# Kernel optimization log

Measured on AMD Instinct MI355X. Metric: run time of the kernel, lower is better.

Reference implementation:

```python
import jax, jax.numpy as jnp
import numpy as np

B, N, D = 4, 4096, 768
H, DH = 12, 64          # heads, dim_head; inner_dim = H*DH = D
DEPTH = 4
HID = int(D * 4.0)      # mlp hidden
LN_EPS = 1e-5


def setup_inputs() -> dict:
    key = jax.random.key(0)
    ks = jax.random.split(key, 7)
    s = 0.02
    return {
        "x": jax.random.normal(ks[0], (B, N, D), jnp.float32),
        "ln1_g": jnp.ones((DEPTH, D), jnp.float32),
        "ln1_b": jnp.zeros((DEPTH, D), jnp.float32),
        "qkv_w": jax.random.normal(ks[1], (DEPTH, D, H * DH), jnp.float32) * s,
        "temp": jnp.ones((DEPTH, H, 1), jnp.float32),
        "out_w": jax.random.normal(ks[2], (DEPTH, H * DH, D), jnp.float32) * s,
        "out_b": jnp.zeros((DEPTH, D), jnp.float32),
        "ln2_g": jnp.ones((DEPTH, D), jnp.float32),
        "ln2_b": jnp.zeros((DEPTH, D), jnp.float32),
        "fc1_w": jax.random.normal(ks[3], (DEPTH, D, HID), jnp.float32) * s,
        "fc1_b": jnp.zeros((DEPTH, HID), jnp.float32),
        "fc2_w": jax.random.normal(ks[4], (DEPTH, HID, D), jnp.float32) * s,
        "fc2_b": jnp.zeros((DEPTH, D), jnp.float32),
    }


def _layernorm(x, g, b):
    mu = jnp.mean(x, axis=-1, keepdims=True)
    var = jnp.mean((x - mu) ** 2, axis=-1, keepdims=True)
    return (x - mu) * jax.lax.rsqrt(var + LN_EPS) * g + b


def _tss_attention(h, qkv_w, temp, out_w, out_b):
    b, n, d = h.shape
    w = h @ qkv_w                                   # (b, n, H*DH)
    w = w.reshape(b, n, H, DH).transpose(0, 2, 1, 3)  # (b, h, n, d)
    # F.normalize over token dim (dim=-2), eps=1e-12
    nrm = jnp.sqrt(jnp.sum(w * w, axis=2, keepdims=True))
    w_normed = w / jnp.maximum(nrm, 1e-12)
    logits = jnp.sum(w_normed * w_normed, axis=-1) * temp[None]  # (b, h, n)
    Pi = jax.nn.softmax(logits, axis=-1)
    Pi_n = Pi / (jnp.sum(Pi, axis=-1, keepdims=True) + 1e-8)
    dots = jnp.einsum('bhn,bhnd->bhd', Pi_n, w * w)[:, :, None, :]  # (b, h, 1, d)
    attn = 1.0 / (1.0 + dots)
    out = -(w * Pi[..., None]) * attn               # (b, h, n, d)
    out = out.transpose(0, 2, 1, 3).reshape(b, n, H * DH)
    return out @ out_w + out_b


def reference(x, ln1_g, ln1_b, qkv_w, temp, out_w, out_b,
              ln2_g, ln2_b, fc1_w, fc1_b, fc2_w, fc2_b):
    for i in range(DEPTH):
        h = _layernorm(x, ln1_g[i], ln1_b[i])
        x = _tss_attention(h, qkv_w[i], temp[i], out_w[i], out_b[i]) + x
        h2 = _layernorm(x, ln2_g[i], ln2_b[i])
        mlp = jax.nn.gelu(h2 @ fc1_w[i] + fc1_b[i], approximate=False) @ fc2_w[i] + fc2_b[i]
        x = mlp + x
    return x
```

## Files before the change

### kernel.cpp

```cpp
#include <hip/hip_runtime.h>
#include <cstdint>
#include <cstddef>

static constexpr int Bc = 4, Nc = 4096, Dc = 768, Hc = 12, DHc = 64;
static constexpr int HIDc = 3072, DEPTHc = 4;
static constexpr int Mc = Bc * Nc;
static constexpr int BHc = Bc * Hc;
static constexpr int BHDc = BHc * DHc;

typedef unsigned short u16;
typedef __bf16 bf16x8 __attribute__((ext_vector_type(8)));
typedef float  f32x4  __attribute__((ext_vector_type(4)));

#define DEV __device__ __forceinline__

DEV u16 f2bf(float x) {
    uint32_t u = __float_as_uint(x);
    u += 0x7fffu + ((u >> 16) & 1u);
    return (u16)(u >> 16);
}
DEV float bf2f(u16 u) { return __uint_as_float(((uint32_t)u) << 16); }
DEV void unp2(uint32_t u, float& a, float& b) {
    a = __uint_as_float(u << 16);
    b = __uint_as_float(u & 0xffff0000u);
}
DEV float gelu_fast(float x) {
    float y = 0.7978845608f * (x + 0.044715f * x * x * x);
    float e = __expf(2.0f * y);
    float t = 1.0f - 2.0f / (e + 1.0f);
    return 0.5f * x * (1.0f + t);
}

DEV void ldg_lds16(const void* g, void* l) {
    __builtin_amdgcn_global_load_lds(
        (const __attribute__((address_space(1))) uint32_t*)(uintptr_t)g,
        (__attribute__((address_space(3))) uint32_t*)(uint32_t)(uintptr_t)l,
        16, 0, 0);
}

__global__ void detect_kernel(const uint32_t* __restrict__ x, uint32_t* __restrict__ flag) {
    int t = threadIdx.x;
    uint32_t w = x[t];
    int e = (w >> 7) & 0xFF;
    __shared__ int cnt[256];
    cnt[t] = (e >= 100 && e <= 140) ? 1 : 0;
    __syncthreads();
    for (int s = 128; s; s >>= 1) {
        if (t < s) cnt[t] += cnt[t + s];
        __syncthreads();
    }
    if (t == 0) flag[0] = (cnt[0] >= 128) ? 1u : 0u;
}

__global__ __launch_bounds__(256) void sentinel_kernel(u16* __restrict__ out, int n) {
    int i = blockIdx.x * 256 + threadIdx.x;
    if (i < n) out[i] = 0x449A;
}

__global__ __launch_bounds__(256) void cvt_param_kernel(
    const void* __restrict__ src, float* __restrict__ dst, int n,
    const uint32_t* __restrict__ flag) {
    int i = blockIdx.x * 256 + threadIdx.x;
    if (i >= n) return;
    if (flag[0]) dst[i] = bf2f(((const u16*)src)[i]);
    else         dst[i] = ((const float*)src)[i];
}

__global__ __launch_bounds__(256) void transpose_cvt_off(
    const void* __restrict__ src, size_t eoff, u16* __restrict__ dst,
    int R, int C, const uint32_t* __restrict__ flag) {
    __shared__ u16 tile[32][33];
    const bool isbf = (flag[0] != 0);
    int c0 = blockIdx.x * 32, r0 = blockIdx.y * 32;
    int tx = threadIdx.x & 31, ty = threadIdx.x >> 5;
#pragma unroll
    for (int j = 0; j < 32; j += 8) {
        size_t off = eoff + (size_t)(r0 + ty + j) * C + (c0 + tx);
        tile[ty + j][tx] = isbf ? ((const u16*)src)[off] : f2bf(((const float*)src)[off]);
    }
    __syncthreads();
#pragma unroll
    for (int j = 0; j < 32; j += 8)
        dst[(size_t)(c0 + ty + j) * R + (r0 + tx)] = tile[tx][ty + j];
}

__global__ __launch_bounds__(256) void ln_kernel(
    const float* __restrict__ x, const float* __restrict__ g,
    const float* __restrict__ bta, u16* __restrict__ out) {
    int row = blockIdx.x, t = threadIdx.x;
    const float* xr = x + (size_t)row * Dc;
    float v0 = xr[t], v1 = xr[t + 256], v2 = xr[t + 512];
    float s = v0 + v1 + v2;
    float ss = v0 * v0 + v1 * v1 + v2 * v2;
    __shared__ float red[8];
    for (int m = 32; m; m >>= 1) { s += __shfl_xor(s, m, 64); ss += __shfl_xor(ss, m, 64); }
    int wave = t >> 6, lane = t & 63;
    if (lane == 0) { red[wave] = s; red[4 + wave] = ss; }
    __syncthreads();
    s  = red[0] + red[1] + red[2] + red[3];
    ss = red[4] + red[5] + red[6] + red[7];
    float mu = s * (1.0f / Dc);
    float var = ss * (1.0f / Dc) - mu * mu;
    float rs = rsqrtf(var + 1e-5f);
    u16* orow = out + (size_t)row * Dc;
    orow[t]       = f2bf((v0 - mu) * rs * g[t]       + bta[t]);
    orow[t + 256] = f2bf((v1 - mu) * rs * g[t + 256] + bta[t + 256]);
    orow[t + 512] = f2bf((v2 - mu) * rs * g[t + 512] + bta[t + 512]);
}

template <int MODE>
__global__ __launch_bounds__(512, 2) void gemm_kernel(
    const u16* __restrict__ A, const u16* __restrict__ Bt,
    float* Cf, u16* Cb, const float* __restrict__ bias, const float* res,
    float* aux, int M, int N, int K) {
    __shared__ __attribute__((aligned(16))) u16 lds[2][2][2][256 * 32];
    const int tid = threadIdx.x;
    const int wave = tid >> 6, lane = tid & 63;
    const int wm = wave >> 2, wn = wave & 3;
    const int bm = blockIdx.y * 256, bn = blockIdx.x * 256;
    const int NKS = K >> 6;

    u16* Lm = &lds[0][0][0][0];
    const u16* L = Lm;

    const int schunk = (lane & 3) ^ ((lane >> 3) & 3);
    const u16* ag = A  + (size_t)(bm + wave * 16 + (lane >> 2)) * K + schunk * 8;
    const u16* bg = Bt + (size_t)(bn + wave * 16 + (lane >> 2)) * K + schunk * 8;
    const size_t jstep = (size_t)128 * K;

    const int fm = lane & 15, fc = lane >> 4;
    const int chunk = (fc ^ ((fm >> 1) & 3)) * 8;
    const int aE0 = (wm * 128 + fm) * 32 + chunk;
    const int aE1 = 8192 + aE0;
    const int bE0 = 32768 + (wn * 64 + fm) * 32 + chunk;
    const int bE1 = 8192 + bE0;

    f32x4 acc[8][4] = {};
    bf16x8 afr[8], bq[2], bq2[2];

#define STG(OP, GB, SS, DD, KH)                                              \
    {   const u16* g_ = GB + (size_t)(SS) * 64 + (KH) * 32;                  \
        u16* d_ = Lm + (OP) * 32768 + (DD) * 16384 + (KH) * 8192 + wave * 512; \
        ldg_lds16(g_, d_);                                                   \
        ldg_lds16(g_ + jstep, d_ + 4096); }

#define MF2(NB, BQ)                                                          \
    __builtin_amdgcn_s_setprio(1);                                           \
    _Pragma("unroll")                                                        \
    for (int m = 0; m < 8; ++m) {                                            \
        acc[m][(NB)]     = __builtin_amdgcn_mfma_f32_16x16x32_bf16(          \
            afr[m], BQ[0], acc[m][(NB)], 0, 0, 0);                           \
        acc[m][(NB) + 1] = __builtin_amdgcn_mfma_f32_16x16x32_bf16(          \
            afr[m], BQ[1], acc[m][(NB) + 1], 0, 0, 0);                       \
    }                                                                        \
    __builtin_amdgcn_s_setprio(0);

#define SYNC                                                                 \
    __builtin_amdgcn_s_barrier();                                            \
    asm volatile("s_waitcnt lgkmcnt(0)" ::: "memory");                       \
    __builtin_amdgcn_sched_barrier(0);

#define VM4 asm volatile("s_waitcnt vmcnt(4)" ::: "memory");

#define KSTEP(D, SS1) {                                                      \
    \
    _Pragma("unroll")                                                        \
    for (int m = 0; m < 8; ++m)                                              \
        afr[m] = *(const bf16x8*)(L + (D) * 16384 + aE0 + m * 512);          \
    bq[0] = *(const bf16x8*)(L + (D) * 16384 + bE0);                         \
    bq[1] = *(const bf16x8*)(L + (D) * 16384 + bE0 + 512);                   \
    STG(0, ag, SS1, (D) ^ 1, 0);                                             \
    SYNC;                                                                    \
    MF2(0, bq);                                                              \
    \
    bq2[0] = *(const bf16x8*)(L + (D) * 16384 + bE0 + 1024);                 \
    bq2[1] = *(const bf16x8*)(L + (D) * 16384 + bE0 + 1536);                 \
    STG(1, bg, SS1, (D) ^ 1, 0);                                             \
    VM4;                                                                     \
    SYNC;                                                                    \
    MF2(2, bq2);                                                             \
    \
    _Pragma("unroll")                                                        \
    for (int m = 0; m < 8; ++m)                                              \
        afr[m] = *(const bf16x8*)(L + (D) * 16384 + aE1 + m * 512);          \
    bq2[0] = *(const bf16x8*)(L + (D) * 16384 + bE1 + 1024);                 \
    bq2[1] = *(const bf16x8*)(L + (D) * 16384 + bE1 + 1536);                 \
    STG(0, ag, SS1, (D) ^ 1, 1);                                             \
    SYNC;                                                                    \
    MF2(2, bq2);                                                             \
    \
    bq[0] = *(const bf16x8*)(L + (D) * 16384 + bE1);                         \
    bq[1] = *(const bf16x8*)(L + (D) * 16384 + bE1 + 512);                   \
    STG(1, bg, SS1, (D) ^ 1, 1);                                             \
    VM4;                                                                     \
    SYNC;                                                                    \
    MF2(0, bq);                                                              \
}

    STG(0, ag, 0, 0, 0);
    STG(1, bg, 0, 0, 0);
    STG(0, ag, 0, 0, 1);
    STG(1, bg, 0, 0, 1);
    asm volatile("s_waitcnt vmcnt(4)" ::: "memory");
    __builtin_amdgcn_s_barrier();
    __builtin_amdgcn_sched_barrier(0);

    for (int s = 0; s < NKS; s += 2) {
        KSTEP(0, s + 1);
        const int s2 = (s + 2 < NKS) ? s + 2 : 0;
        KSTEP(1, s2);
    }
    asm volatile("s_waitcnt vmcnt(0)" ::: "memory");

#undef KSTEP
#undef VM4
#undef SYNC
#undef MF2
#undef STG

    const int er = (lane >> 4) * 4;
    const int ec = lane & 15;
    float csq[4] = {0.f, 0.f, 0.f, 0.f};
#pragma unroll
    for (int mf = 0; mf < 8; ++mf) {
        const int row0 = bm + wm * 128 + mf * 16 + er;
#pragma unroll
        for (int nf = 0; nf < 4; ++nf) {
            const int col = bn + wn * 64 + nf * 16 + ec;
#pragma unroll
            for (int r = 0; r < 4; ++r) {
                const size_t off = (size_t)(row0 + r) * N + col;
                float v = acc[mf][nf][r];
                if (MODE == 1) {
                    Cf[off] = v + bias[col] + res[off];
                } else if (MODE == 2) {
                    Cb[off] = f2bf(gelu_fast(v + bias[col]));
                } else {
                    Cb[off] = f2bf(v);
                    csq[nf] += v * v;
                }
            }
        }
    }
    if (MODE == 3) {
        const int b = bm >> 12;
#pragma unroll
        for (int nf = 0; nf < 4; ++nf) {
            float s = csq[nf];
            s += __shfl_xor(s, 16, 64);
            s += __shfl_xor(s, 32, 64);
            if (lane < 16) {
                const int col = bn + wn * 64 + nf * 16 + lane;
                const int bh = b * Hc + (col >> 6);
                atomicAdd(&aux[bh * DHc + (col & 63)], s);
            }
        }
    }
}

__global__ __launch_bounds__(256) void logits_kernel(
    const u16* __restrict__ w, const float* __restrict__ nrm2,
    const float* __restrict__ tp, float* __restrict__ logits) {
    int blk = blockIdx.x;
    int chunk = blk & 15, bh = blk >> 4;
    int b = bh / Hc, h = bh - b * Hc;
    int t = threadIdx.x, dq = t & 3, nr = t >> 2;
    __shared__ float inv[64];
    if (t < 64) inv[t] = 1.0f / fmaxf(nrm2[bh * DHc + t], 1e-24f);
    __syncthreads();
    float tl = tp[h];
#pragma unroll
    for (int jj = 0; jj < 4; jj++) {
        int n = chunk * 256 + jj * 64 + nr;
        const uint4* wr = (const uint4*)(w + ((size_t)b * Nc + n) * Dc + h * DHc + dq * 16);
        uint4 u0 = wr[0], u1 = wr[1];
        float acc = 0.f;
        float e0, e1;
        const float* iv = inv + dq * 16;
        unp2(u0.x, e0, e1); acc += e0 * e0 * iv[0]  + e1 * e1 * iv[1];
        unp2(u0.y, e0, e1); acc += e0 * e0 * iv[2]  + e1 * e1 * iv[3];
        unp2(u0.z, e0, e1); acc += e0 * e0 * iv[4]  + e1 * e1 * iv[5];
        unp2(u0.w, e0, e1); acc += e0 * e0 * iv[6]  + e1 * e1 * iv[7];
        unp2(u1.x, e0, e1); acc += e0 * e0 * iv[8]  + e1 * e1 * iv[9];
        unp2(u1.y, e0, e1); acc += e0 * e0 * iv[10] + e1 * e1 * iv[11];
        unp2(u1.z, e0, e1); acc += e0 * e0 * iv[12] + e1 * e1 * iv[13];
        unp2(u1.w, e0, e1); acc += e0 * e0 * iv[14] + e1 * e1 * iv[15];
        acc += __shfl_xor(acc, 1, 64);
        acc += __shfl_xor(acc, 2, 64);
        if (dq == 0) logits[(size_t)bh * Nc + n] = tl * acc;
    }
}

__global__ __launch_bounds__(256) void softmax_kernel(
    const float* __restrict__ logits, float* __restrict__ Pi, float* __restrict__ rowsc) {
    int bh = blockIdx.x, t = threadIdx.x;
    int wave = t >> 6, lane = t & 63;
    const float4* lg = (const float4*)(logits + (size_t)bh * Nc);
    float4 v[4];
    float mx = -3.4e38f;
    __shared__ float red[4];
#pragma unroll
    for (int j = 0; j < 4; j++) {
        v[j] = lg[t + 256 * j];
        mx = fmaxf(mx, fmaxf(fmaxf(v[j].x, v[j].y), fmaxf(v[j].z, v[j].w)));
    }
    for (int m = 32; m; m >>= 1) mx = fmaxf(mx, __shfl_xor(mx, m, 64));
    if (lane == 0) red[wave] = mx;
    __syncthreads();
    mx = fmaxf(fmaxf(red[0], red[1]), fmaxf(red[2], red[3]));
    __syncthreads();
    float s = 0.f;
#pragma unroll
    for (int j = 0; j < 4; j++) {
        v[j].x = expf(v[j].x - mx); v[j].y = expf(v[j].y - mx);
        v[j].z = expf(v[j].z - mx); v[j].w = expf(v[j].w - mx);
        s += v[j].x + v[j].y + v[j].z + v[j].w;
    }
    for (int m = 32; m; m >>= 1) s += __shfl_xor(s, m, 64);
    if (lane == 0) red[wave] = s;
    __syncthreads();
    s = red[0] + red[1] + red[2] + red[3];
    __syncthreads();
    float invs = 1.0f / s;
    float s2 = 0.f;
    float4* Pr = (float4*)(Pi + (size_t)bh * Nc);
#pragma unroll
    for (int j = 0; j < 4; j++) {
        float4 p;
        p.x = v[j].x * invs; p.y = v[j].y * invs;
        p.z = v[j].z * invs; p.w = v[j].w * invs;
        s2 += p.x + p.y + p.z + p.w;
        Pr[t + 256 * j] = p;
    }
    for (int m = 32; m; m >>= 1) s2 += __shfl_xor(s2, m, 64);
    if (lane == 0) red[wave] = s2;
    __syncthreads();
    if (t == 0) rowsc[bh] = 1.0f / (red[0] + red[1] + red[2] + red[3] + 1e-8f);
}

__global__ __launch_bounds__(256) void dots_kernel(
    const u16* __restrict__ w, const float* __restrict__ Pi,
    const float* __restrict__ rowsc, float* __restrict__ dots) {
    int blk = blockIdx.x;
    int chunk = blk & 15, bh = blk >> 4;
    int b = bh / Hc, h = bh - b * Hc;
    int t = threadIdx.x, d4 = t & 15, rg = t >> 4;
    const u16* base = w + ((size_t)b * Nc + chunk * 256 + rg) * Dc + h * DHc + d4 * 4;
    const float* Prow = Pi + (size_t)bh * Nc + chunk * 256 + rg;
    float4 acc = {0.f, 0.f, 0.f, 0.f};
#pragma unroll 4
    for (int j = 0; j < 16; j++) {
        uint2 u = *(const uint2*)(base + (size_t)j * 16 * Dc);
        float p = Prow[j * 16];
        float a0, a1, a2, a3;
        unp2(u.x, a0, a1); unp2(u.y, a2, a3);
        acc.x += p * a0 * a0; acc.y += p * a1 * a1;
        acc.z += p * a2 * a2; acc.w += p * a3 * a3;
    }
    __shared__ float4 red[256];
    red[t] = acc;
    __syncthreads();
    if (t < 64) {
        float s = 0.f;
#pragma unroll
        for (int r = 0; r < 16; r++) {
            const float* f = (const float*)&red[r * 16 + (t >> 2)];
            s += f[t & 3];
        }
        atomicAdd(&dots[bh * DHc + t], s * rowsc[bh]);
    }
}

__global__ __launch_bounds__(256) void attnout_kernel(
    const u16* __restrict__ w, const float* __restrict__ Pi,
    const float* __restrict__ dots, u16* __restrict__ out) {
    int idx = blockIdx.x * 256 + threadIdx.x;
    int cg = idx % (Dc / 8);
    int m = idx / (Dc / 8);
    int b = m >> 12, n = m & 4095;
    int c = cg * 8, h = c >> 6, d = c & 63;
    int bh = b * Hc + h;
    uint4 wv = ((const uint4*)w)[idx];
    float pi = Pi[(size_t)bh * Nc + n];
    float4 dv0 = *(const float4*)(dots + bh * DHc + d);
    float4 dv1 = *(const float4*)(dots + bh * DHc + d + 4);
    float a0, a1, a2, a3, a4, a5, a6, a7;
    unp2(wv.x, a0, a1); unp2(wv.y, a2, a3);
    unp2(wv.z, a4, a5); unp2(wv.w, a6, a7);
    union { u16 u[8]; uint4 v4; } pk;
    pk.u[0] = f2bf(-(a0 * pi) / (1.0f + dv0.x));
    pk.u[1] = f2bf(-(a1 * pi) / (1.0f + dv0.y));
    pk.u[2] = f2bf(-(a2 * pi) / (1.0f + dv0.z));
    pk.u[3] = f2bf(-(a3 * pi) / (1.0f + dv0.w));
    pk.u[4] = f2bf(-(a4 * pi) / (1.0f + dv1.x));
    pk.u[5] = f2bf(-(a5 * pi) / (1.0f + dv1.y));
    pk.u[6] = f2bf(-(a6 * pi) / (1.0f + dv1.z));
    pk.u[7] = f2bf(-(a7 * pi) / (1.0f + dv1.w));
    ((uint4*)out)[idx] = pk.v4;
}

extern "C" void kernel_launch(void* const* d_in, const int* in_sizes, int n_in,
                              void* d_out, int out_size, void* d_ws, size_t ws_size,
                              hipStream_t stream) {
    const void* x_in = d_in[0];
    const void* ln1g = d_in[1];
    const void* ln1b = d_in[2];
    const void* qkvw = d_in[3];
    const void* temp = d_in[4];
    const void* outw = d_in[5];
    const void* outb = d_in[6];
    const void* ln2g = d_in[7];
    const void* ln2b = d_in[8];
    const void* fc1w = d_in[9];
    const void* fc1b = d_in[10];
    const void* fc2w = d_in[11];
    const void* fc2b = d_in[12];

    char* p = (char*)d_ws;
    auto alloc = [&](size_t bytes) {
        void* r = (void*)p;
        p += (bytes + 255) & ~(size_t)255;
        return r;
    };
    float* xbuf = (float*)alloc((size_t)Mc * Dc * 4);
    void*  big  = alloc((size_t)Mc * HIDc * 2);
    u16*   wbuf = (u16*)big;
    u16*   gbuf = (u16*)big;
    u16*  abuf  = (u16*)alloc((size_t)Mc * Dc * 2);
    const size_t QKV_T = (size_t)Dc * Dc, OUT_T = (size_t)Dc * Dc;
    const size_t FC1_T = (size_t)HIDc * Dc, FC2_T = (size_t)Dc * HIDc;
    const size_t LSTRIDE = QKV_T + OUT_T + FC1_T + FC2_T;
    u16*  wTL   = (u16*)alloc(LSTRIDE * 2);
    float* nrm2 = (float*)alloc((size_t)BHDc * 4);
    float* dots = (float*)alloc((size_t)BHDc * 4);
    float* logit = (float*)alloc((size_t)BHc * Nc * 4);
    float* Pi    = (float*)alloc((size_t)BHc * Nc * 4);
    float* rowsc = (float*)alloc((size_t)BHc * 4);
    uint32_t* flag = (uint32_t*)alloc(256);
    float* ln1g_f = (float*)alloc((size_t)DEPTHc * Dc * 4);
    float* ln1b_f = (float*)alloc((size_t)DEPTHc * Dc * 4);
    float* ln2g_f = (float*)alloc((size_t)DEPTHc * Dc * 4);
    float* ln2b_f = (float*)alloc((size_t)DEPTHc * Dc * 4);
    float* outb_f = (float*)alloc((size_t)DEPTHc * Dc * 4);
    float* fc1b_f = (float*)alloc((size_t)DEPTHc * HIDc * 4);
    float* fc2b_f = (float*)alloc((size_t)DEPTHc * Dc * 4);
    float* temp_f = (float*)alloc((size_t)DEPTHc * Hc * 4);
    if ((size_t)(p - (char*)d_ws) > ws_size) {
        sentinel_kernel<<<(out_size + 255) / 256, 256, 0, stream>>>((u16*)d_out, out_size);
        return;
    }

    detect_kernel<<<1, 256, 0, stream>>>((const uint32_t*)x_in, flag);

    auto cvt = [&](const void* s, float* d, int n) {
        cvt_param_kernel<<<(n + 255) / 256, 256, 0, stream>>>(s, d, n, flag);
    };
    cvt(x_in, xbuf, Mc * Dc);
    cvt(ln1g, ln1g_f, DEPTHc * Dc);
    cvt(ln1b, ln1b_f, DEPTHc * Dc);
    cvt(ln2g, ln2g_f, DEPTHc * Dc);
    cvt(ln2b, ln2b_f, DEPTHc * Dc);
    cvt(outb, outb_f, DEPTHc * Dc);
    cvt(fc1b, fc1b_f, DEPTHc * HIDc);
    cvt(fc2b, fc2b_f, DEPTHc * Dc);
    cvt(temp, temp_f, DEPTHc * Hc);

    u16* qkvT = wTL;
    u16* outT = qkvT + QKV_T;
    u16* fc1T = outT + OUT_T;
    u16* fc2T = fc1T + FC1_T;

    for (int i = 0; i < DEPTHc; i++) {
        transpose_cvt_off<<<dim3(Dc / 32, Dc / 32), 256, 0, stream>>>(
            qkvw, (size_t)i * Dc * Dc, qkvT, Dc, Dc, flag);
        transpose_cvt_off<<<dim3(Dc / 32, Dc / 32), 256, 0, stream>>>(
            outw, (size_t)i * Dc * Dc, outT, Dc, Dc, flag);
        transpose_cvt_off<<<dim3(HIDc / 32, Dc / 32), 256, 0, stream>>>(
            fc1w, (size_t)i * Dc * HIDc, fc1T, Dc, HIDc, flag);
        transpose_cvt_off<<<dim3(Dc / 32, HIDc / 32), 256, 0, stream>>>(
            fc2w, (size_t)i * HIDc * Dc, fc2T, HIDc, Dc, flag);

        ln_kernel<<<Mc, 256, 0, stream>>>(xbuf, ln1g_f + i * Dc, ln1b_f + i * Dc, abuf);
        hipMemsetAsync(nrm2, 0, (size_t)2 * BHDc * 4, stream);
        gemm_kernel<3><<<dim3(Dc / 256, Mc / 256), 512, 0, stream>>>(
            abuf, qkvT, nullptr, wbuf, nullptr, nullptr, nrm2, Mc, Dc, Dc);
        logits_kernel<<<BHc * 16, 256, 0, stream>>>(wbuf, nrm2, temp_f + i * Hc, logit);
        softmax_kernel<<<BHc, 256, 0, stream>>>(logit, Pi, rowsc);
        dots_kernel<<<BHc * 16, 256, 0, stream>>>(wbuf, Pi, rowsc, dots);
        attnout_kernel<<<(Mc * Dc / 8) / 256, 256, 0, stream>>>(wbuf, Pi, dots, abuf);
        gemm_kernel<1><<<dim3(Dc / 256, Mc / 256), 512, 0, stream>>>(
            abuf, outT, xbuf, nullptr, outb_f + i * Dc, xbuf, nullptr, Mc, Dc, Dc);
        ln_kernel<<<Mc, 256, 0, stream>>>(xbuf, ln2g_f + i * Dc, ln2b_f + i * Dc, abuf);
        gemm_kernel<2><<<dim3(HIDc / 256, Mc / 256), 512, 0, stream>>>(
            abuf, fc1T, nullptr, gbuf, fc1b_f + i * HIDc, nullptr, nullptr, Mc, HIDc, Dc);
        gemm_kernel<1><<<dim3(Dc / 256, Mc / 256), 512, 0, stream>>>(
            gbuf, fc2T, xbuf, nullptr, fc2b_f + i * Dc, xbuf, nullptr, Mc, Dc, HIDc);
    }
    hipMemcpyAsync(d_out, xbuf, (size_t)Mc * Dc * 4, hipMemcpyDeviceToDevice, stream);
}
```

Measured before the change: 1.712 ms.

## Restructure GEMM k-step into two subphases with fewer barriers

Replaces the four-phase k-step, which had a barrier and an lgkmcnt wait before each pair of MFMA groups, with two subphases. Each subphase loads all A and B fragments, issues both A and B global-to-LDS stages, runs a full 8x4 MFMA block, and then waits and hits a barrier. This halves the barrier count and removes the explicit sched_barrier and setprio hints, leaving the compiler to interleave instructions. The cost is higher register pressure from holding 4 B fragments at once, and less hand-controlled overlap between loads and MFMAs.

```diff
diff --git a/kernel.cpp b/kernel.cpp
--- a/kernel.cpp
+++ b/kernel.cpp
@@ -136,7 +136,6 @@
     const int bE1 = 8192 + bE0;
 
     f32x4 acc[8][4] = {};
-    bf16x8 afr[8], bq[2], bq2[2];
 
 #define STG(OP, GB, SS, DD, KH)                                              \
     {   const u16* g_ = GB + (size_t)(SS) * 64 + (KH) * 32;                  \
@@ -144,58 +143,30 @@
         ldg_lds16(g_, d_);                                                   \
         ldg_lds16(g_ + jstep, d_ + 4096); }
 
-#define MF2(NB, BQ)                                                          \
-    __builtin_amdgcn_s_setprio(1);                                           \
+#define SUBPHASE(D, AE, BE, S1, KH) {                                        \
+    bf16x8 af_[8], b_[4];                                                    \
+    _Pragma("unroll")                                                        \
+    for (int m = 0; m < 8; ++m)                                              \
+        af_[m] = *(const bf16x8*)(L + (D) * 16384 + (AE) + m * 512);         \
+    _Pragma("unroll")                                                        \
+    for (int n = 0; n < 4; ++n)                                              \
+        b_[n] = *(const bf16x8*)(L + (D) * 16384 + (BE) + n * 512);          \
+    STG(0, ag, S1, (D) ^ 1, KH);                                             \
+    STG(1, bg, S1, (D) ^ 1, KH);                                             \
     _Pragma("unroll")                                                        \
     for (int m = 0; m < 8; ++m) {                                            \
-        acc[m][(NB)]     = __builtin_amdgcn_mfma_f32_16x16x32_bf16(          \
-            afr[m], BQ[0], acc[m][(NB)], 0, 0, 0);                           \
-        acc[m][(NB) + 1] = __builtin_amdgcn_mfma_f32_16x16x32_bf16(          \
-            afr[m], BQ[1], acc[m][(NB) + 1], 0, 0, 0);                       \
+        acc[m][0] = __builtin_amdgcn_mfma_f32_16x16x32_bf16(af_[m], b_[0], acc[m][0], 0, 0, 0); \
+        acc[m][1] = __builtin_amdgcn_mfma_f32_16x16x32_bf16(af_[m], b_[1], acc[m][1], 0, 0, 0); \
+        acc[m][2] = __builtin_amdgcn_mfma_f32_16x16x32_bf16(af_[m], b_[2], acc[m][2], 0, 0, 0); \
+        acc[m][3] = __builtin_amdgcn_mfma_f32_16x16x32_bf16(af_[m], b_[3], acc[m][3], 0, 0, 0); \
     }                                                                        \
-    __builtin_amdgcn_s_setprio(0);
-
-#define SYNC                                                                 \
+    asm volatile("s_waitcnt vmcnt(4)" ::: "memory");                         \
     __builtin_amdgcn_s_barrier();                                            \
-    asm volatile("s_waitcnt lgkmcnt(0)" ::: "memory");                       \
-    __builtin_amdgcn_sched_barrier(0);
-
-#define VM4 asm volatile("s_waitcnt vmcnt(4)" ::: "memory");
-
-#define KSTEP(D, SS1) {                                                      \
-    \
-    _Pragma("unroll")                                                        \
-    for (int m = 0; m < 8; ++m)                                              \
-        afr[m] = *(const bf16x8*)(L + (D) * 16384 + aE0 + m * 512);          \
-    bq[0] = *(const bf16x8*)(L + (D) * 16384 + bE0);                         \
-    bq[1] = *(const bf16x8*)(L + (D) * 16384 + bE0 + 512);                   \
-    STG(0, ag, SS1, (D) ^ 1, 0);                                             \
-    SYNC;                                                                    \
-    MF2(0, bq);                                                              \
-    \
-    bq2[0] = *(const bf16x8*)(L + (D) * 16384 + bE0 + 1024);                 \
-    bq2[1] = *(const bf16x8*)(L + (D) * 16384 + bE0 + 1536);                 \
-    STG(1, bg, SS1, (D) ^ 1, 0);                                             \
-    VM4;                                                                     \
-    SYNC;                                                                    \
-    MF2(2, bq2);                                                             \
-    \
-    _Pragma("unroll")                                                        \
-    for (int m = 0; m < 8; ++m)                                              \
-        afr[m] = *(const bf16x8*)(L + (D) * 16384 + aE1 + m * 512);          \
-    bq2[0] = *(const bf16x8*)(L + (D) * 16384 + bE1 + 1024);                 \
-    bq2[1] = *(const bf16x8*)(L + (D) * 16384 + bE1 + 1536);                 \
-    STG(0, ag, SS1, (D) ^ 1, 1);                                             \
-    SYNC;                                                                    \
-    MF2(2, bq2);                                                             \
-    \
-    bq[0] = *(const bf16x8*)(L + (D) * 16384 + bE1);                         \
-    bq[1] = *(const bf16x8*)(L + (D) * 16384 + bE1 + 512);                   \
-    STG(1, bg, SS1, (D) ^ 1, 1);                                             \
-    VM4;                                                                     \
-    SYNC;                                                                    \
-    MF2(0, bq);                                                              \
-}
+}
+
+#define KSTEP(D, S1)                                                         \
+    SUBPHASE(D, aE0, bE0, S1, 0);                                            \
+    SUBPHASE(D, aE1, bE1, S1, 1);
 
     STG(0, ag, 0, 0, 0);
     STG(1, bg, 0, 0, 0);
@@ -203,7 +174,6 @@
     STG(1, bg, 0, 0, 1);
     asm volatile("s_waitcnt vmcnt(4)" ::: "memory");
     __builtin_amdgcn_s_barrier();
-    __builtin_amdgcn_sched_barrier(0);
 
     for (int s = 0; s < NKS; s += 2) {
         KSTEP(0, s + 1);
@@ -213,9 +183,7 @@
     asm volatile("s_waitcnt vmcnt(0)" ::: "memory");
 
 #undef KSTEP
-#undef VM4
-#undef SYNC
-#undef MF2
+#undef SUBPHASE
 #undef STG
 
     const int er = (lane >> 4) * 4;
```

Result: faster. 1.640 ms (-4.2%).
